# Kernel tuning notes

Measured on AMD Instinct MI355X. Metric: run time of the kernel, lower is better.

Reference implementation:

```python
import jax, jax.numpy as jnp
import numpy as np

POOLED_H, POOLED_W = 7, 7
SPATIAL_SCALE = 0.25
SAMPLING_RATIO = 2  # fixed > 0, so exactly sr x sr grid points per bin


def setup_inputs() -> dict:
    key = jax.random.key(0)
    k1, k2, k3, k4 = jax.random.split(key, 4)
    N, C, H, W = 4, 256, 200, 200
    K = 1000
    feature = jax.random.normal(k1, (N, C, H, W), dtype=jnp.float32)
    # rois in this module's convention: (batch_idx, y1, x1, y2, x2) in IMAGE coords
    # (image is 800x800 since spatial_scale = 0.25 -> 200x200 feature map)
    b = jax.random.randint(k2, (K,), 0, N).astype(jnp.float32)
    yx1 = jax.random.uniform(k3, (K, 2), minval=0.0, maxval=700.0)
    wh = jax.random.uniform(k4, (K, 2), minval=20.0, maxval=100.0)
    yx2 = jnp.clip(yx1 + wh, 0.0, 800.0)
    rois = jnp.concatenate([b[:, None], yx1[:, :1], yx1[:, 1:], yx2[:, :1], yx2[:, 1:]], axis=1)
    return {"feature": feature, "rois": rois}


def _axis_prep(coord, size):
    """coord: [K, G] continuous sample coords along one axis of length `size`.
    Returns low/high integer indices and (masked) lerp weights, matching the
    torchvision/detectron bilinear_interpolate edge handling (aligned=False)."""
    valid = ((coord >= -1.0) & (coord <= size)).astype(coord.dtype)
    c = jnp.maximum(coord, 0.0)
    c0 = jnp.minimum(jnp.floor(c).astype(jnp.int32), size - 1)
    c1 = jnp.minimum(c0 + 1, size - 1)
    l = jnp.where(c0 >= size - 1, 0.0, c - c0.astype(c.dtype))
    h = 1.0 - l
    return c0, c1, l * valid, h * valid


def _roi_align_2d(feature, rois_tv):
    # rois_tv: [K,5] = (batch, x1, y1, x2, y2) in torchvision order
    N, C, H, W = feature.shape
    K = rois_tv.shape[0]
    sr = SAMPLING_RATIO
    GH, GW = POOLED_H * sr, POOLED_W * sr
    b = rois_tv[:, 0].astype(jnp.int32)
    x1 = rois_tv[:, 1] * SPATIAL_SCALE
    y1 = rois_tv[:, 2] * SPATIAL_SCALE
    x2 = rois_tv[:, 3] * SPATIAL_SCALE
    y2 = rois_tv[:, 4] * SPATIAL_SCALE
    roi_w = jnp.maximum(x2 - x1, 1.0)
    roi_h = jnp.maximum(y2 - y1, 1.0)
    bin_w = roi_w / POOLED_W  # [K]
    bin_h = roi_h / POOLED_H
    # per-axis sample grid offsets (in units of bins): bin + (i+0.5)/sr
    gw = jnp.arange(GW) // sr + (jnp.arange(GW) % sr + 0.5) / sr  # [GW]
    gh = jnp.arange(GH) // sr + (jnp.arange(GH) % sr + 0.5) / sr  # [GH]
    xs = x1[:, None] + gw[None, :] * bin_w[:, None]  # [K, GW]
    ys = y1[:, None] + gh[None, :] * bin_h[:, None]  # [K, GH]
    x0, x1i, lx, hx = _axis_prep(xs, W)
    y0, y1i, ly, hy = _axis_prep(ys, H)

    def gather(yc, xc):
        # -> [K, GH, GW, C]
        return feature[b[:, None, None], :, yc[:, :, None], xc[:, None, :]]

    # bilinear: weights are separable in y and x
    wy_hi = hy[:, :, None, None]  # [K,GH,1,1]
    wy_lo = ly[:, :, None, None]
    wx_hi = hx[:, None, :, None]  # [K,1,GW,1]
    wx_lo = lx[:, None, :, None]
    val = (wy_hi * wx_hi * gather(y0, x0)
           + wy_hi * wx_lo * gather(y0, x1i)
           + wy_lo * wx_hi * gather(y1i, x0)
           + wy_lo * wx_lo * gather(y1i, x1i))  # [K, GH, GW, C]
    # average the sr x sr samples per bin
    out = val.reshape(K, POOLED_H, sr, POOLED_W, sr, C).mean(axis=(2, 4))
    return jnp.transpose(out, (0, 3, 1, 2))  # [K, C, PH, PW]


def reference(feature, rois):
    # module forward: permute (b, y1, x1, y2, x2) -> (b, x1, y1, x2, y2)
    rois_tv = rois[:, jnp.array([0, 2, 1, 4, 3])]
    return _roi_align_2d(feature, rois_tv)
```

## Files before the change

### kernel.cpp

```cpp
#include <hip/hip_runtime.h>


constexpr int POOLED = 7;
constexpr int C_DIM = 256;
constexpr int H_DIM = 200;
constexpr int W_DIM = 200;
constexpr int HW    = H_DIM * W_DIM;
constexpr float SCALE = 0.25f;

constexpr int PROWS = 26;
constexpr int PSTR  = 36;

struct alignas(16) RoiParams {
    float bw, bh, x1, y1;
    int   k, rx0a, ry0, nrw;
};

__device__ __forceinline__ RoiParams compute_params(const float* __restrict__ rois, int k)
{
    const float* r = rois + (size_t)k * 5;
    RoiParams p;
    const float y1 = r[1] * SCALE;
    const float x1 = r[2] * SCALE;
    const float y2 = r[3] * SCALE;
    const float x2 = r[4] * SCALE;
    p.bw = fmaxf(x2 - x1, 1.0f) * (1.0f / POOLED);
    p.bh = fmaxf(y2 - y1, 1.0f) * (1.0f / POOLED);
    p.x1 = x1;
    p.y1 = y1;
    p.k  = k;
    const int n   = (int)r[0];
    const int rx0 = (int)fmaf(0.25f, p.bw, x1);
    const int ry0 = (int)fmaf(0.25f, p.bh, y1);
    const int rx1 = (int)fmaf(6.75f, p.bw, x1);
    const int ry1 = (int)fmaf(6.75f, p.bh, y1);
    p.rx0a = rx0 & ~3;
    p.ry0  = ry0;
    const int R  = ry1 - ry0 + 1;
    const int w4 = ((rx1 + 1 - p.rx0a) >> 2) + 1;
    p.nrw = (n << 16) | (R << 8) | w4;
    return p;
}

__global__ __launch_bounds__(1024) void roi_prep_sort(
    const float* __restrict__ rois, RoiParams* __restrict__ pp, int K)
{
    __shared__ unsigned skey[1024];
    const int tid = threadIdx.x;

    unsigned key = 0xFFFFFFFFu;
    if (tid < K) {
        const float* r = rois + (size_t)tid * 5;
        const int n  = (int)r[0];
        const int qy = (min(max((int)(r[1] * SCALE), 0), H_DIM - 1)) >> 1;
        const int qx = (min(max((int)(r[2] * SCALE), 0), W_DIM - 1)) >> 1;
        unsigned my = (unsigned)qy, mx = (unsigned)qx;
        my = (my | (my << 4)) & 0x0F0Fu; my = (my | (my << 2)) & 0x3333u; my = (my | (my << 1)) & 0x5555u;
        mx = (mx | (mx << 4)) & 0x0F0Fu; mx = (mx | (mx << 2)) & 0x3333u; mx = (mx | (mx << 1)) & 0x5555u;
        const unsigned mort = (my << 1) | mx;
        key = ((((unsigned)n << 16) | mort) << 10) | (unsigned)tid;
    }
    skey[tid] = key;
    __syncthreads();

    for (int sz = 2; sz <= 1024; sz <<= 1) {
        for (int st = sz >> 1; st > 0; st >>= 1) {
            const int p = tid ^ st;
            const unsigned a = skey[tid], b = skey[p];
            __syncthreads();
            const bool up = (tid & sz) == 0;
            const unsigned lo = min(a, b), hi = max(a, b);
            skey[tid] = (tid < p) ? (up ? lo : hi) : (up ? hi : lo);
            __syncthreads();
        }
    }

    if (tid < K) pp[tid] = compute_params(rois, (int)(skey[tid] & 1023u));
}

template <bool SORTED>
__global__ __launch_bounds__(256, 5) void roi_align_v6(
    const float* __restrict__ feat,
    const float* __restrict__ rois,
    const RoiParams* __restrict__ pp,
    float* __restrict__ out,
    int K, int KperX)
{
    __shared__ float patch[8][PROWS][PSTR];

    RoiParams p;
    int cg;
    if (SORTED) {
        const int bid = blockIdx.x;
        const int xcd = bid & 7;
        const int j   = bid >> 3;
        const int rr  = j % KperX;
        cg            = j / KperX;
        const int rank = xcd * KperX + rr;
        if (rank >= K) return;
        p = pp[rank];
    } else {
        cg = blockIdx.y;
        p = compute_params(rois, blockIdx.x);
    }

    const int w    = threadIdx.x >> 6;
    const int lane = threadIdx.x & 63;
    const int c0   = cg * 8 + w * 2;
    const int n    = p.nrw >> 16;
    const int R    = (p.nrw >> 8) & 255;
    const int w4   = p.nrw & 255;

    const float* plane0 = feat + ((size_t)n * C_DIM + c0) * (size_t)HW;
    {
        const int ly = lane >> 3;
        const int lx = lane & 7;
        const int col4 = p.rx0a + lx * 4;
        const int lb   = min(col4, W_DIM - 4);
        const bool hi  = col4 > W_DIM - 4;
        const bool con = lx < w4;

        int  roff[4];
        bool on[4];
        #pragma unroll
        for (int i = 0; i < 4; ++i) {
            const int rr2 = ly + 8 * i;
            on[i]   = con && (rr2 <= R);
            roff[i] = min(p.ry0 + rr2, H_DIM - 1) * W_DIM + lb;
        }
        float4 v0[4], v1[4];
        #pragma unroll
        for (int i = 0; i < 4; ++i)
            if (on[i]) v0[i] = *reinterpret_cast<const float4*>(plane0 + roff[i]);
        #pragma unroll
        for (int i = 0; i < 4; ++i)
            if (on[i]) v1[i] = *reinterpret_cast<const float4*>(plane0 + HW + roff[i]);
        #pragma unroll
        for (int i = 0; i < 4; ++i) {
            if (on[i]) {
                float4 t = v0[i];
                if (hi) { t.x = t.w; t.y = t.w; t.z = t.w; }
                *reinterpret_cast<float4*>(&patch[w * 2 + 0][ly + 8 * i][lx * 4]) = t;
                t = v1[i];
                if (hi) { t.x = t.w; t.y = t.w; t.z = t.w; }
                *reinterpret_cast<float4*>(&patch[w * 2 + 1][ly + 8 * i][lx * 4]) = t;
            }
        }
    }

    if (lane < POOLED * POOLED) {
        const int ph = (lane * 37) >> 8;
        const int pw = lane - ph * 7;

        float wx[2][2], wy[2][2];
        int   xr[2], yr[2];
        #pragma unroll
        for (int i = 0; i < 2; ++i) {
            const float fi = 0.25f + 0.5f * (float)i;
            float xs = fmaf((float)pw + fi, p.bw, p.x1);
            int   a0 = (int)xs;
            const float l = xs - (float)a0;
            wx[i][0] = 1.0f - l;
            wx[i][1] = l;
            xr[i] = a0 - p.rx0a;
            float ys = fmaf((float)ph + fi, p.bh, p.y1);
            int   b0 = (int)ys;
            const float m = ys - (float)b0;
            wy[i][0] = (1.0f - m) * 0.25f;
            wy[i][1] = m * 0.25f;
            yr[i] = b0 - p.ry0;
        }
        float cw[2][2][2][2];
        #pragma unroll
        for (int iy = 0; iy < 2; ++iy)
            #pragma unroll
            for (int ix = 0; ix < 2; ++ix)
                #pragma unroll
                for (int dy = 0; dy < 2; ++dy)
                    #pragma unroll
                    for (int dx = 0; dx < 2; ++dx)
                        cw[iy][ix][dy][dx] = wy[iy][dy] * wx[ix][dx];

        const size_t obase = ((size_t)p.k * C_DIM + c0) * (POOLED * POOLED) + lane;
        #pragma unroll
        for (int pc = 0; pc < 2; ++pc) {
            float acc = 0.0f;
            #pragma unroll
            for (int iy = 0; iy < 2; ++iy) {
                #pragma unroll
                for (int ix = 0; ix < 2; ++ix) {
                    const int y0 = yr[iy], x0 = xr[ix];
                    acc = fmaf(cw[iy][ix][0][0], patch[w * 2 + pc][y0][x0],         acc);
                    acc = fmaf(cw[iy][ix][0][1], patch[w * 2 + pc][y0][x0 + 1],     acc);
                    acc = fmaf(cw[iy][ix][1][0], patch[w * 2 + pc][y0 + 1][x0],     acc);
                    acc = fmaf(cw[iy][ix][1][1], patch[w * 2 + pc][y0 + 1][x0 + 1], acc);
                }
            }
            out[obase + (size_t)pc * (POOLED * POOLED)] = acc;
        }
    }
}

extern "C" void kernel_launch(void* const* d_in, const int* in_sizes, int n_in,
                              void* d_out, int out_size, void* d_ws, size_t ws_size,
                              hipStream_t stream) {
    const float* feature = (const float*)d_in[0];
    const float* rois    = (const float*)d_in[1];
    float* out = (float*)d_out;

    const int K = in_sizes[1] / 5;

    if (K <= 1024 && ws_size >= sizeof(RoiParams) * (size_t)K) {
        RoiParams* pp = (RoiParams*)d_ws;
        roi_prep_sort<<<1, 1024, 0, stream>>>(rois, pp, K);
        const int KperX = (K + 7) / 8;
        const int blocks = 8 * KperX * (C_DIM / 8);
        roi_align_v6<true><<<blocks, 256, 0, stream>>>(feature, rois, pp, out, K, KperX);
    } else {
        dim3 grid(K, C_DIM / 8);
        roi_align_v6<false><<<grid, 256, 0, stream>>>(feature, rois, nullptr, out, K, 0);
    }
}
```

Baseline: 68.95 us.

## Precompute x-direction interpolation per row into compact LDS before y-pass

Replaces the full patch of raw feature rows in shared memory with a separable two-pass scheme. Threads gather the two x-neighbours for each of the 14 x sample columns per row, lerp them in x, and store a compact float2 (two channels) per sample in a swizzled LDS array. The pooling stage then only does y-interpolation with two float4 LDS reads per sample row. Shared memory shrinks and launch bounds rise to 8 blocks per CU for more occupancy. The cost is scalar, uncoalesced global loads in place of float4 row loads, plus index arithmetic per sample.

Result: slower. 81.75 us (+18.6%).

```diff
diff --git a/kernel.cpp b/kernel.cpp
--- a/kernel.cpp
+++ b/kernel.cpp
@@ -8,12 +8,12 @@
 constexpr int HW    = H_DIM * W_DIM;
 constexpr float SCALE = 0.25f;
 
-constexpr int PROWS = 26;
-constexpr int PSTR  = 36;
+constexpr int GROWS = 26;
+constexpr int GSTR  = 16;
 
 struct alignas(16) RoiParams {
     float bw, bh, x1, y1;
-    int   k, rx0a, ry0, nrw;
+    int   k, ry0, nR, unused;
 };
 
 __device__ __forceinline__ RoiParams compute_params(const float* __restrict__ rois, int k)
@@ -30,15 +30,12 @@
     p.y1 = y1;
     p.k  = k;
     const int n   = (int)r[0];
-    const int rx0 = (int)fmaf(0.25f, p.bw, x1);
     const int ry0 = (int)fmaf(0.25f, p.bh, y1);
-    const int rx1 = (int)fmaf(6.75f, p.bw, x1);
     const int ry1 = (int)fmaf(6.75f, p.bh, y1);
-    p.rx0a = rx0 & ~3;
-    p.ry0  = ry0;
-    const int R  = ry1 - ry0 + 1;
-    const int w4 = ((rx1 + 1 - p.rx0a) >> 2) + 1;
-    p.nrw = (n << 16) | (R << 8) | w4;
+    p.ry0 = ry0;
+    const int R = ry1 - ry0 + 1;
+    p.nR = (n << 8) | R;
+    p.unused = 0;
     return p;
 }
 
@@ -65,12 +62,12 @@
 
     for (int sz = 2; sz <= 1024; sz <<= 1) {
         for (int st = sz >> 1; st > 0; st >>= 1) {
-            const int p = tid ^ st;
-            const unsigned a = skey[tid], b = skey[p];
+            const int pr = tid ^ st;
+            const unsigned a = skey[tid], b = skey[pr];
             __syncthreads();
             const bool up = (tid & sz) == 0;
             const unsigned lo = min(a, b), hi = max(a, b);
-            skey[tid] = (tid < p) ? (up ? lo : hi) : (up ? hi : lo);
+            skey[tid] = (tid < pr) ? (up ? lo : hi) : (up ? hi : lo);
             __syncthreads();
         }
     }
@@ -79,14 +76,14 @@
 }
 
 template <bool SORTED>
-__global__ __launch_bounds__(256, 5) void roi_align_v6(
+__global__ __launch_bounds__(256, 8) void roi_align_v8(
     const float* __restrict__ feat,
     const float* __restrict__ rois,
     const RoiParams* __restrict__ pp,
     float* __restrict__ out,
     int K, int KperX)
 {
-    __shared__ float patch[8][PROWS][PSTR];
+    __shared__ float2 g2[4][GROWS][GSTR];
 
     RoiParams p;
     int cg;
@@ -107,43 +104,51 @@
     const int w    = threadIdx.x >> 6;
     const int lane = threadIdx.x & 63;
     const int c0   = cg * 8 + w * 2;
-    const int n    = p.nrw >> 16;
-    const int R    = (p.nrw >> 8) & 255;
-    const int w4   = p.nrw & 255;
-
+    const int n    = p.nR >> 8;
+    const int R    = p.nR & 255;
     const float* plane0 = feat + ((size_t)n * C_DIM + c0) * (size_t)HW;
-    {
-        const int ly = lane >> 3;
-        const int lx = lane & 7;
-        const int col4 = p.rx0a + lx * 4;
-        const int lb   = min(col4, W_DIM - 4);
-        const bool hi  = col4 > W_DIM - 4;
-        const bool con = lx < w4;
-
-        int  roff[4];
-        bool on[4];
+
+    const int P = 14 * (R + 1);
+    #pragma unroll
+    for (int ch = 0; ch < 2; ++ch) {
+        float vv[3][4];
+        float lw[3];
+        bool  on[3];
         #pragma unroll
-        for (int i = 0; i < 4; ++i) {
-            const int rr2 = ly + 8 * i;
-            on[i]   = con && (rr2 <= R);
-            roff[i] = min(p.ry0 + rr2, H_DIM - 1) * W_DIM + lb;
-        }
-        float4 v0[4], v1[4];
+        for (int j = 0; j < 3; ++j) {
+            const int jj = ch * 3 + j;
+            if (jj * 64 < P) {
+                const int i = jj * 64 + lane;
+                const int r = (i * 9363) >> 17;
+                const int s = i - r * 14;
+                const float xs = fmaf(fmaf(0.5f, (float)s, 0.25f), p.bw, p.x1);
+                const int   x0 = (int)xs;
+                lw[j] = xs - (float)x0;
+                const int fr = min(p.ry0 + r, H_DIM - 1);
+                const int i0 = fr * W_DIM + x0;
+                const int i1 = i0 + (x0 < W_DIM - 1 ? 1 : 0);
+                on[j] = i < P;
+                if (on[j]) {
+                    vv[j][0] = plane0[i0];
+                    vv[j][1] = plane0[i1];
+                    vv[j][2] = plane0[HW + i0];
+                    vv[j][3] = plane0[HW + i1];
+                }
+            }
+        }
         #pragma unroll
-        for (int i = 0; i < 4; ++i)
-            if (on[i]) v0[i] = *reinterpret_cast<const float4*>(plane0 + roff[i]);
-        #pragma unroll
-        for (int i = 0; i < 4; ++i)
-            if (on[i]) v1[i] = *reinterpret_cast<const float4*>(plane0 + HW + roff[i]);
-        #pragma unroll
-        for (int i = 0; i < 4; ++i) {
-            if (on[i]) {
-                float4 t = v0[i];
-                if (hi) { t.x = t.w; t.y = t.w; t.z = t.w; }
-                *reinterpret_cast<float4*>(&patch[w * 2 + 0][ly + 8 * i][lx * 4]) = t;
-                t = v1[i];
-                if (hi) { t.x = t.w; t.y = t.w; t.z = t.w; }
-                *reinterpret_cast<float4*>(&patch[w * 2 + 1][ly + 8 * i][lx * 4]) = t;
+        for (int j = 0; j < 3; ++j) {
+            const int jj = ch * 3 + j;
+            if (jj * 64 < P) {
+                const int i = jj * 64 + lane;
+                if (on[j]) {
+                    const int r  = (i * 9363) >> 17;
+                    const int s  = i - r * 14;
+                    const int sc = s ^ ((r & 3) << 2);
+                    g2[w][r][sc] = make_float2(
+                        fmaf(lw[j], vv[j][1] - vv[j][0], vv[j][0]),
+                        fmaf(lw[j], vv[j][3] - vv[j][2], vv[j][2]));
+                }
             }
         }
     }
@@ -152,52 +157,32 @@
         const int ph = (lane * 37) >> 8;
         const int pw = lane - ph * 7;
 
-        float wx[2][2], wy[2][2];
-        int   xr[2], yr[2];
+        float acc0 = 0.0f, acc1 = 0.0f;
         #pragma unroll
-        for (int i = 0; i < 2; ++i) {
-            const float fi = 0.25f + 0.5f * (float)i;
-            float xs = fmaf((float)pw + fi, p.bw, p.x1);
-            int   a0 = (int)xs;
-            const float l = xs - (float)a0;
-            wx[i][0] = 1.0f - l;
-            wx[i][1] = l;
-            xr[i] = a0 - p.rx0a;
-            float ys = fmaf((float)ph + fi, p.bh, p.y1);
-            int   b0 = (int)ys;
-            const float m = ys - (float)b0;
-            wy[i][0] = (1.0f - m) * 0.25f;
-            wy[i][1] = m * 0.25f;
-            yr[i] = b0 - p.ry0;
-        }
-        float cw[2][2][2][2];
-        #pragma unroll
-        for (int iy = 0; iy < 2; ++iy)
-            #pragma unroll
-            for (int ix = 0; ix < 2; ++ix)
-                #pragma unroll
-                for (int dy = 0; dy < 2; ++dy)
-                    #pragma unroll
-                    for (int dx = 0; dx < 2; ++dx)
-                        cw[iy][ix][dy][dx] = wy[iy][dy] * wx[ix][dx];
+        for (int iy = 0; iy < 2; ++iy) {
+            const float fi = 0.25f + 0.5f * (float)iy;
+            const float ys = fmaf((float)ph + fi, p.bh, p.y1);
+            const int   b0 = (int)ys;
+            const float m  = ys - (float)b0;
+            const float hy = (1.0f - m) * 0.25f;
+            const float ly = m * 0.25f;
+            const int y0 = b0 - p.ry0;
+
+            const int sc0 = (2 * pw) ^ ((y0 & 3) << 2);
+            const float4 va = *reinterpret_cast<const float4*>(&g2[w][y0][sc0]);
+            const int y1r = y0 + 1;
+            const int sc1 = (2 * pw) ^ ((y1r & 3) << 2);
+            const float4 vb = *reinterpret_cast<const float4*>(&g2[w][y1r][sc1]);
+
+            acc0 = fmaf(hy, va.x + va.z, acc0);
+            acc1 = fmaf(hy, va.y + va.w, acc1);
+            acc0 = fmaf(ly, vb.x + vb.z, acc0);
+            acc1 = fmaf(ly, vb.y + vb.w, acc1);
+        }
 
         const size_t obase = ((size_t)p.k * C_DIM + c0) * (POOLED * POOLED) + lane;
-        #pragma unroll
-        for (int pc = 0; pc < 2; ++pc) {
-            float acc = 0.0f;
-            #pragma unroll
-            for (int iy = 0; iy < 2; ++iy) {
-                #pragma unroll
-                for (int ix = 0; ix < 2; ++ix) {
-                    const int y0 = yr[iy], x0 = xr[ix];
-                    acc = fmaf(cw[iy][ix][0][0], patch[w * 2 + pc][y0][x0],         acc);
-                    acc = fmaf(cw[iy][ix][0][1], patch[w * 2 + pc][y0][x0 + 1],     acc);
-                    acc = fmaf(cw[iy][ix][1][0], patch[w * 2 + pc][y0 + 1][x0],     acc);
-                    acc = fmaf(cw[iy][ix][1][1], patch[w * 2 + pc][y0 + 1][x0 + 1], acc);
-                }
-            }
-            out[obase + (size_t)pc * (POOLED * POOLED)] = acc;
-        }
+        out[obase]                     = acc0;
+        out[obase + (POOLED * POOLED)] = acc1;
     }
 }
 
@@ -215,9 +200,9 @@
         roi_prep_sort<<<1, 1024, 0, stream>>>(rois, pp, K);
         const int KperX = (K + 7) / 8;
         const int blocks = 8 * KperX * (C_DIM / 8);
-        roi_align_v6<true><<<blocks, 256, 0, stream>>>(feature, rois, pp, out, K, KperX);
+        roi_align_v8<true><<<blocks, 256, 0, stream>>>(feature, rois, pp, out, K, KperX);
     } else {
         dim3 grid(K, C_DIM / 8);
-        roi_align_v6<false><<<grid, 256, 0, stream>>>(feature, rois, nullptr, out, K, 0);
-    }
-}
+        roi_align_v8<false><<<grid, 256, 0, stream>>>(feature, rois, nullptr, out, K, 0);
+    }
+}
```
